# Performance work log

Hardware: AMD Instinct MI355X
Metric: run time of the kernel (lower is better)

Reference implementation:

```python
import jax, jax.numpy as jnp
import numpy as np

MIDC = 128
HEADS = 8
HEADC = MIDC // HEADS
EPS = 1e-5


def setup_inputs() -> dict:
    key = jax.random.key(0)
    ks = jax.random.split(key, 7)
    B, C, H, W = 8, MIDC, 128, 128
    x = jax.random.normal(ks[0], (B, C, H, W), dtype=jnp.float32)
    s = 1.0 / np.sqrt(C)
    qkv_w = jax.random.normal(ks[1], (3 * C, C), dtype=jnp.float32) * s
    qkv_b = jnp.zeros((3 * C,), dtype=jnp.float32)
    o1_w = jax.random.normal(ks[2], (C, C), dtype=jnp.float32) * s
    o1_b = jnp.zeros((C,), dtype=jnp.float32)
    o2_w = jax.random.normal(ks[3], (C, C), dtype=jnp.float32) * s
    o2_b = jnp.zeros((C,), dtype=jnp.float32)
    kln_w = jnp.ones((HEADS, 1, HEADC), dtype=jnp.float32)
    kln_b = jnp.zeros((HEADS, 1, HEADC), dtype=jnp.float32)
    vln_w = jnp.ones((HEADS, 1, HEADC), dtype=jnp.float32)
    vln_b = jnp.zeros((HEADS, 1, HEADC), dtype=jnp.float32)
    return {"x": x, "qkv_w": qkv_w, "qkv_b": qkv_b, "o1_w": o1_w, "o1_b": o1_b,
            "o2_w": o2_w, "o2_b": o2_b, "kln_w": kln_w, "kln_b": kln_b,
            "vln_w": vln_w, "vln_b": vln_b}


def _layernorm(t, w, b):
    # torch LayerNorm clone: mean/std over last dim, std uses ddof=1 (unbiased)
    mean = t.mean(-1, keepdims=True)
    std = jnp.std(t, axis=-1, ddof=1, keepdims=True)
    return w * ((t - mean) / (std + EPS)) + b


def reference(x, qkv_w, qkv_b, o1_w, o1_b, o2_w, o2_b, kln_w, kln_b, vln_w, vln_b):
    B, C, H, W = x.shape
    N = H * W
    bias0 = x
    # 1x1 conv == pointwise linear over channels
    xf = x.transpose(0, 2, 3, 1).reshape(B, N, C)              # [B, N, C]
    qkv = xf @ qkv_w.T + qkv_b                                 # [B, N, 3C]
    qkv = qkv.reshape(B, N, HEADS, 3 * HEADC).transpose(0, 2, 1, 3)  # [B, h, N, 3d]
    q, k, v = jnp.split(qkv, 3, axis=-1)                       # each [B, h, N, d]
    k = _layernorm(k, kln_w, kln_b)
    v = _layernorm(v, vln_w, vln_b)
    kv = jnp.einsum('bhnd,bhne->bhde', k, v) / N               # [B, h, d, d]
    av = jnp.einsum('bhnd,bhde->bhne', q, kv)                  # [B, h, N, d]
    av = av.transpose(0, 2, 1, 3).reshape(B, H, W, C)
    ret = av.transpose(0, 3, 1, 2) + bias0                     # [B, C, H, W]
    # o_proj1 -> GELU -> o_proj2, residual
    rf = ret.transpose(0, 2, 3, 1)                             # [B, H, W, C]
    h1 = jax.nn.gelu(rf @ o1_w.T + o1_b, approximate=False)
    h2 = h1 @ o2_w.T + o2_b
    return h2.transpose(0, 3, 1, 2) + bias0
```

## Files before the change

### kernel.cpp

```cpp
#include <hip/hip_runtime.h>
#include <hip/hip_bf16.h>

#define LN_EPS 1e-5f

typedef __bf16 bf16x8 __attribute__((ext_vector_type(8)));
typedef float  f32x4  __attribute__((ext_vector_type(4)));
typedef unsigned short u16;
typedef unsigned int u32;

__device__ __forceinline__ u16 f2bf(float f) {
    __bf16 b = (__bf16)f;
    return __builtin_bit_cast(u16, b);
}
__device__ __forceinline__ bf16x8 zero8() {
    bf16x8 v;
#pragma unroll
    for (int j = 0; j < 8; j++) v[j] = (__bf16)0.f;
    return v;
}
__device__ __forceinline__ float gelu_f(float v) {
    float t = v * fmaf(v * v, 0.0713548162726f, 1.5957691216057f);
    return v / (1.f + __expf(-t));
}

__global__ __launch_bounds__(256) void prep_kernel(
    const float* __restrict__ qkv_w, const float* __restrict__ o1_w,
    const float* __restrict__ o2_w, u16* __restrict__ wq,
    u16* __restrict__ o1f, u16* __restrict__ o2f) {
    int i = blockIdx.x * 256 + threadIdx.x;
    if (i >= 81920) return;
    int j = i;
    const float* src;
    u16* dst;
    if (j < 49152) { src = qkv_w; dst = wq; }
    else if (j < 65536) { j -= 49152; src = o1_w; dst = o1f; }
    else { j -= 65536; src = o2_w; dst = o2f; }
    int jj = j & 7;
    int l  = (j >> 3) & 63;
    int s  = (j >> 9) & 3;
    int t  = j >> 11;
    int outc = t * 16 + (l & 15);
    int k    = s * 32 + ((l >> 4) & 3) * 8 + jj;
    dst[j] = f2bf(src[outc * 128 + k]);
}

__global__ __launch_bounds__(512, 6) void k1(
    const float* __restrict__ x, const u16* __restrict__ wq,
    const float* __restrict__ qkv_b,
    const float* __restrict__ klw, const float* __restrict__ klb,
    const float* __restrict__ vlw, const float* __restrict__ vlb,
    u16* __restrict__ q_ws, float* __restrict__ part) {
    __shared__ __align__(16) char Rbuf[51200];
    u16* x_a  = (u16*)Rbuf;
    u16* kv_s = (u16*)Rbuf;
    u16* q_s  = (u16*)(Rbuf + 33792);
    u16* kT   = (u16*)Rbuf;
    u16* vT   = (u16*)(Rbuf + 18432);

    const int tid  = threadIdx.x;
    const int lane = tid & 63;
    const int wv   = tid >> 6;
    const int stripe = wv >> 1;
    const int half   = wv & 1;
    const int bid  = blockIdx.x;
    const int b    = bid >> 8;
    const int n0   = (bid & 255) * 64;

    {
        int cw  = tid & 63;
        int sub = tid >> 6;
        const float* p0 = x + ((size_t)(b * 128 + 2 * cw)) * 16384 + n0 + sub * 8;
        const float* p1 = p0 + 16384;
        float4 a0 = ((const float4*)p0)[0], a1 = ((const float4*)p0)[1];
        float4 c0 = ((const float4*)p1)[0], c1 = ((const float4*)p1)[1];
        float av[8] = {a0.x, a0.y, a0.z, a0.w, a1.x, a1.y, a1.z, a1.w};
        float cv[8] = {c0.x, c0.y, c0.z, c0.w, c1.x, c1.y, c1.z, c1.w};
        u32* dst = (u32*)x_a;
#pragma unroll
        for (int j = 0; j < 8; j++)
            dst[(sub * 8 + j) * 68 + cw] = (u32)f2bf(av[j]) | ((u32)f2bf(cv[j]) << 16);
    }
    __syncthreads();

    const int m16  = stripe * 16;
    const int l15  = lane & 15;
    const int quad = lane >> 4;

    bf16x8 af[4];
#pragma unroll
    for (int s = 0; s < 4; s++)
        af[s] = *(const bf16x8*)&x_a[(m16 + l15) * 136 + s * 32 + quad * 8];
    __syncthreads();

    const int tb = half * 12;
#pragma unroll
    for (int hh = 0; hh < 4; hh++) {
        const int tq = tb + 3 * hh;
        f32x4 aq  = (f32x4){0.f, 0.f, 0.f, 0.f};
        f32x4 ak  = (f32x4){0.f, 0.f, 0.f, 0.f};
        f32x4 avv = (f32x4){0.f, 0.f, 0.f, 0.f};
#pragma unroll
        for (int s = 0; s < 4; s++) {
            bf16x8 bq = *(const bf16x8*)(wq + (size_t)(((tq + 0) * 4 + s) * 64 + lane) * 8);
            bf16x8 bk = *(const bf16x8*)(wq + (size_t)(((tq + 1) * 4 + s) * 64 + lane) * 8);
            bf16x8 bv = *(const bf16x8*)(wq + (size_t)(((tq + 2) * 4 + s) * 64 + lane) * 8);
            aq  = __builtin_amdgcn_mfma_f32_16x16x32_bf16(af[s], bq, aq, 0, 0, 0);
            ak  = __builtin_amdgcn_mfma_f32_16x16x32_bf16(af[s], bk, ak, 0, 0, 0);
            avv = __builtin_amdgcn_mfma_f32_16x16x32_bf16(af[s], bv, avv, 0, 0, 0);
        }
        const int h = half * 4 + hh;
        float biasq = qkv_b[(tq + 0) * 16 + l15];
        float biask = qkv_b[(tq + 1) * 16 + l15];
        float biasv = qkv_b[(tq + 2) * 16 + l15];
#pragma unroll
        for (int r = 0; r < 4; r++) {
            int row = m16 + quad * 4 + r;
            q_s[row * 136 + h * 16 + l15]       = f2bf(aq[r] + biasq);
            kv_s[row * 264 + h * 32 + l15]      = f2bf(ak[r] + biask);
            kv_s[row * 264 + h * 32 + 16 + l15] = f2bf(avv[r] + biasv);
        }
    }
    __syncthreads();

    {
#pragma unroll
        for (int p = 0; p < 2; p++) {
            int c = tid + p * 512;
            int lane_c = c & 63;
            int s  = (c >> 6) & 3;
            int tl = c >> 8;
            int row = tl * 16 + (lane_c & 15);
            const uint4* src = (const uint4*)&q_s[row * 136 + s * 32 + (lane_c >> 4) * 8];
            size_t gtile = (size_t)b * 1024 + (n0 >> 4) + tl;
            *(uint4*)(q_ws + gtile * 2048 + s * 512 + lane_c * 8) = *src;
        }
    }
    const int hL = __builtin_amdgcn_readfirstlane(wv);
    const u16* rowp = &kv_s[lane * 264 + hL * 32];
    bf16x8 rk0 = *(const bf16x8*)(rowp);
    bf16x8 rk1 = *(const bf16x8*)(rowp + 8);
    bf16x8 rv0 = *(const bf16x8*)(rowp + 16);
    bf16x8 rv1 = *(const bf16x8*)(rowp + 24);
    __syncthreads();

    {
        float kf[16], vf[16];
#pragma unroll
        for (int j = 0; j < 8; j++) {
            kf[j] = (float)rk0[j]; kf[8 + j] = (float)rk1[j];
            vf[j] = (float)rv0[j]; vf[8 + j] = (float)rv1[j];
        }
        float ksum = 0.f, ksq = 0.f, vsum = 0.f, vsq = 0.f;
#pragma unroll
        for (int d = 0; d < 16; d++) {
            ksum += kf[d]; ksq = fmaf(kf[d], kf[d], ksq);
            vsum += vf[d]; vsq = fmaf(vf[d], vf[d], vsq);
        }
        float km = ksum * (1.f / 16.f);
        float kvar = (ksq - 16.f * km * km) * (1.f / 15.f);
        kvar = kvar < 0.f ? 0.f : kvar;
        float kinv = 1.f / (sqrtf(kvar) + LN_EPS);
        float vm = vsum * (1.f / 16.f);
        float vvar = (vsq - 16.f * vm * vm) * (1.f / 15.f);
        vvar = vvar < 0.f ? 0.f : vvar;
        float vinv = 1.f / (sqrtf(vvar) + LN_EPS);
        const float* kwp = klw + hL * 16; const float* kbp = klb + hL * 16;
        const float* vwp = vlw + hL * 16; const float* vbp = vlb + hL * 16;
#pragma unroll
        for (int d = 0; d < 16; d++) {
            kT[(hL * 16 + d) * 72 + lane] = f2bf(fmaf((kf[d] - km) * kinv, kwp[d], kbp[d]));
            vT[(hL * 16 + d) * 72 + lane] = f2bf(fmaf((vf[d] - vm) * vinv, vwp[d], vbp[d]));
        }
    }
    __syncthreads();

    {
        const u16* ka = &kT[(hL * 16 + l15) * 72 + quad * 8];
        const u16* vb = &vT[(hL * 16 + l15) * 72 + quad * 8];
        bf16x8 A0 = *(const bf16x8*)(ka);
        bf16x8 A1 = *(const bf16x8*)(ka + 32);
        bf16x8 B0 = *(const bf16x8*)(vb);
        bf16x8 B1 = *(const bf16x8*)(vb + 32);
        f32x4 kv = __builtin_amdgcn_mfma_f32_16x16x32_bf16(A0, B0, (f32x4){0.f,0.f,0.f,0.f}, 0, 0, 0);
        kv = __builtin_amdgcn_mfma_f32_16x16x32_bf16(A1, B1, kv, 0, 0, 0);
        ((f32x4*)part)[(size_t)(bid * 8 + hL) * 64 + lane] = kv;
    }
}

__global__ __launch_bounds__(256) void k_red(const float* __restrict__ part,
                                             u16* __restrict__ kvf) {
    __shared__ f32x4 red[4][64];
    const int tid  = threadIdx.x;
    const int lane = tid & 63;
    const int wvq  = tid >> 6;
    const int b = blockIdx.x >> 3;
    const int h = blockIdx.x & 7;

    const f32x4* p = (const f32x4*)part;
    f32x4 s = (f32x4){0.f, 0.f, 0.f, 0.f};
#pragma unroll 8
    for (int tt = 0; tt < 64; tt++) {
        int t = wvq * 64 + tt;
        f32x4 v = p[((size_t)(b * 256 + t) * 8 + h) * 64 + lane];
        s += v;
    }
    red[wvq][lane] = s;
    __syncthreads();
    if (tid < 64) {
        f32x4 tot = red[0][lane];
#pragma unroll
        for (int w = 1; w < 4; w++) tot += red[w][lane];
#pragma unroll
        for (int r = 0; r < 4; r++) {
            int dk = (lane >> 4) * 4 + r;
            int dv = lane & 15;
            kvf[(size_t)(b * 8 + h) * 256 + (dk >> 3) * 128 + dv * 8 + (dk & 7)] =
                f2bf(tot[r] * (1.f / 16384.f));
        }
    }
}

__global__ __launch_bounds__(256, 5) void k2(
    const float* __restrict__ x, const u16* __restrict__ q_ws,
    const u16* __restrict__ kvf, const u16* __restrict__ o1f,
    const u16* __restrict__ o2f, const float* __restrict__ o1_b,
    const float* __restrict__ o2_b, float* __restrict__ out) {
    __shared__ u16 a_s[32 * 136];
    __shared__ float x_s[128 * 36];

    const int tid  = threadIdx.x;
    const int lane = tid & 63;
    const int wv   = tid >> 6;
    const int stripe = wv >> 1;
    const int half   = wv & 1;
    const int bid  = blockIdx.x;
    const int b    = bid >> 9;
    const int n0   = (bid & 511) * 32;

    const int m16  = stripe * 16;
    const int l15  = lane & 15;
    const int quad = lane >> 4;
    const bool act = quad < 2;

    bf16x8 qf[4], kvb[4];
    {
        size_t gtile = (size_t)b * 1024 + (n0 >> 4) + stripe;
#pragma unroll
        for (int hh = 0; hh < 4; hh++) {
            int h = half * 4 + hh;
            if (act) {
                int laneq = ((h & 1) * 2 + quad) * 16 + l15;
                qf[hh]  = *(const bf16x8*)(q_ws + gtile * 2048 + (h >> 1) * 512 + laneq * 8);
                kvb[hh] = *(const bf16x8*)(kvf + (size_t)(b * 8 + h) * 256 + quad * 128 + l15 * 8);
            } else {
                qf[hh] = zero8(); kvb[hh] = zero8();
            }
        }
    }

    {
        int c = tid >> 1, nh = (tid & 1) * 16;
        const float4* xs = (const float4*)(x + ((size_t)(b * 128 + c)) * 16384 + n0 + nh);
        float4* xd = (float4*)&x_s[c * 36 + nh];
#pragma unroll
        for (int i = 0; i < 4; i++) xd[i] = xs[i];
    }
    __syncthreads();

#pragma unroll
    for (int hh = 0; hh < 4; hh++) {
        int h = half * 4 + hh;
        f32x4 acc = __builtin_amdgcn_mfma_f32_16x16x32_bf16(
            qf[hh], kvb[hh], (f32x4){0.f,0.f,0.f,0.f}, 0, 0, 0);
#pragma unroll
        for (int r = 0; r < 4; r++) {
            float rv = acc[r] + x_s[(h * 16 + l15) * 36 + m16 + quad * 4 + r];
            a_s[(m16 + quad * 4 + r) * 136 + h * 16 + l15] = f2bf(rv);
        }
    }
    __syncthreads();

    bf16x8 af2[4];
#pragma unroll
    for (int s = 0; s < 4; s++)
        af2[s] = *(const bf16x8*)&a_s[(m16 + l15) * 136 + s * 32 + quad * 8];
    f32x4 acc2[4];
#pragma unroll
    for (int t = 0; t < 4; t++) acc2[t] = (f32x4){0.f,0.f,0.f,0.f};
#pragma unroll
    for (int tt = 0; tt < 4; tt++) {
        int t = half * 4 + tt;
#pragma unroll
        for (int s = 0; s < 4; s++) {
            bf16x8 bf = *(const bf16x8*)(o1f + (size_t)((t * 4 + s) * 64 + lane) * 8);
            acc2[tt] = __builtin_amdgcn_mfma_f32_16x16x32_bf16(af2[s], bf, acc2[tt], 0, 0, 0);
        }
    }
    float g[4][4];
#pragma unroll
    for (int tt = 0; tt < 4; tt++) {
        float bb = o1_b[(half * 4 + tt) * 16 + l15];
#pragma unroll
        for (int r = 0; r < 4; r++)
            g[tt][r] = gelu_f(acc2[tt][r] + bb);
    }
    __syncthreads();
#pragma unroll
    for (int tt = 0; tt < 4; tt++)
#pragma unroll
        for (int r = 0; r < 4; r++)
            a_s[(m16 + quad * 4 + r) * 136 + (half * 4 + tt) * 16 + l15] = f2bf(g[tt][r]);
    __syncthreads();

#pragma unroll
    for (int s = 0; s < 4; s++)
        af2[s] = *(const bf16x8*)&a_s[(m16 + l15) * 136 + s * 32 + quad * 8];
#pragma unroll
    for (int t = 0; t < 4; t++) acc2[t] = (f32x4){0.f,0.f,0.f,0.f};
#pragma unroll
    for (int tt = 0; tt < 4; tt++) {
        int t = half * 4 + tt;
#pragma unroll
        for (int s = 0; s < 4; s++) {
            bf16x8 bf = *(const bf16x8*)(o2f + (size_t)((t * 4 + s) * 64 + lane) * 8);
            acc2[tt] = __builtin_amdgcn_mfma_f32_16x16x32_bf16(af2[s], bf, acc2[tt], 0, 0, 0);
        }
    }
#pragma unroll
    for (int tt = 0; tt < 4; tt++) {
        int t = half * 4 + tt;
        float bb = o2_b[t * 16 + l15];
#pragma unroll
        for (int r = 0; r < 4; r++) {
            int row = m16 + quad * 4 + r;
            int col = t * 16 + l15;
            x_s[col * 36 + row] = acc2[tt][r] + bb + x_s[col * 36 + row];
        }
    }
    __syncthreads();

    {
        int c = tid >> 1, nh = (tid & 1) * 16;
        float4* dst = (float4*)(out + ((size_t)(b * 128 + c)) * 16384 + n0 + nh);
        const float4* sv = (const float4*)&x_s[c * 36 + nh];
#pragma unroll
        for (int i = 0; i < 4; i++) dst[i] = sv[i];
    }
}

extern "C" void kernel_launch(void* const* d_in, const int* in_sizes, int n_in,
                              void* d_out, int out_size, void* d_ws, size_t ws_size,
                              hipStream_t stream) {
    (void)in_sizes; (void)n_in; (void)out_size; (void)ws_size;
    const float* x     = (const float*)d_in[0];
    const float* qkv_w = (const float*)d_in[1];
    const float* qkv_b = (const float*)d_in[2];
    const float* o1_w  = (const float*)d_in[3];
    const float* o1_b  = (const float*)d_in[4];
    const float* o2_w  = (const float*)d_in[5];
    const float* o2_b  = (const float*)d_in[6];
    const float* klw   = (const float*)d_in[7];
    const float* klb   = (const float*)d_in[8];
    const float* vlw   = (const float*)d_in[9];
    const float* vlb   = (const float*)d_in[10];
    float* outp = (float*)d_out;

    char* ws = (char*)d_ws;
    u16*   kvf  = (u16*)(ws);
    u16*   wq   = (u16*)(ws + 32768);
    u16*   o1f  = (u16*)(ws + 131072);
    u16*   o2f  = (u16*)(ws + 163840);
    float* part = (float*)(ws + 196608);
    u16*   q_ws = (u16*)(ws + 196608 + 16777216);

    prep_kernel<<<320, 256, 0, stream>>>(qkv_w, o1_w, o2_w, wq, o1f, o2f);
    k1<<<2048, 512, 0, stream>>>(x, wq, qkv_b, klw, klb, vlw, vlb, q_ws, part);
    k_red<<<64, 256, 0, stream>>>(part, kvf);
    k2<<<4096, 256, 0, stream>>>(x, q_ws, kvf, o1f, o2f, o1_b, o2_b, outp);
}
```

Before: 205.5 us.

## Split k1 into two 32-row subtiles per 256-thread block, accumulating kv in registers

The k1 kernel now launches 256-thread blocks that process each 64-row tile as two sequential 32-row subtiles. The per-head k^T v partial is accumulated in MFMA registers across both subtiles, and the LDS staging buffer is halved. The aim is to let more blocks reside per CU and improve latency hiding while keeping the same grid and partial-sum output. The cost is less parallelism inside each block and an extra barrier between subtiles. The LayerNorm work is also remapped so each wave handles two heads.

```diff
diff --git a/kernel.cpp b/kernel.cpp
--- a/kernel.cpp
+++ b/kernel.cpp
@@ -44,27 +44,27 @@
     dst[j] = f2bf(src[outc * 128 + k]);
 }
 
-__global__ __launch_bounds__(512, 6) void k1(
+__device__ __forceinline__ void k1_tile(
     const float* __restrict__ x, const u16* __restrict__ wq,
     const float* __restrict__ qkv_b,
     const float* __restrict__ klw, const float* __restrict__ klb,
     const float* __restrict__ vlw, const float* __restrict__ vlb,
-    u16* __restrict__ q_ws, float* __restrict__ part) {
-    __shared__ __align__(16) char Rbuf[51200];
+    u16* __restrict__ q_ws, char* Rbuf,
+    int b, int n0, f32x4* kvacc) {
     u16* x_a  = (u16*)Rbuf;
     u16* kv_s = (u16*)Rbuf;
-    u16* q_s  = (u16*)(Rbuf + 33792);
+    u16* q_s  = (u16*)(Rbuf + 16896);
     u16* kT   = (u16*)Rbuf;
-    u16* vT   = (u16*)(Rbuf + 18432);
+    u16* vT   = (u16*)(Rbuf + 10240);
 
     const int tid  = threadIdx.x;
     const int lane = tid & 63;
     const int wv   = tid >> 6;
     const int stripe = wv >> 1;
     const int half   = wv & 1;
-    const int bid  = blockIdx.x;
-    const int b    = bid >> 8;
-    const int n0   = (bid & 255) * 64;
+    const int m16  = stripe * 16;
+    const int l15  = lane & 15;
+    const int quad = lane >> 4;
 
     {
         int cw  = tid & 63;
@@ -82,10 +82,6 @@
     }
     __syncthreads();
 
-    const int m16  = stripe * 16;
-    const int l15  = lane & 15;
-    const int quad = lane >> 4;
-
     bf16x8 af[4];
 #pragma unroll
     for (int s = 0; s < 4; s++)
@@ -125,7 +121,7 @@
     {
 #pragma unroll
         for (int p = 0; p < 2; p++) {
-            int c = tid + p * 512;
+            int c = tid + p * 256;
             int lane_c = c & 63;
             int s  = (c >> 6) & 3;
             int tl = c >> 8;
@@ -135,8 +131,9 @@
             *(uint4*)(q_ws + gtile * 2048 + s * 512 + lane_c * 8) = *src;
         }
     }
-    const int hL = __builtin_amdgcn_readfirstlane(wv);
-    const u16* rowp = &kv_s[lane * 264 + hL * 32];
+    const int hL   = wv * 2 + (lane >> 5);
+    const int rown = lane & 31;
+    const u16* rowp = &kv_s[rown * 264 + hL * 32];
     bf16x8 rk0 = *(const bf16x8*)(rowp);
     bf16x8 rk1 = *(const bf16x8*)(rowp + 8);
     bf16x8 rv0 = *(const bf16x8*)(rowp + 16);
@@ -168,22 +165,49 @@
         const float* vwp = vlw + hL * 16; const float* vbp = vlb + hL * 16;
 #pragma unroll
         for (int d = 0; d < 16; d++) {
-            kT[(hL * 16 + d) * 72 + lane] = f2bf(fmaf((kf[d] - km) * kinv, kwp[d], kbp[d]));
-            vT[(hL * 16 + d) * 72 + lane] = f2bf(fmaf((vf[d] - vm) * vinv, vwp[d], vbp[d]));
-        }
-    }
-    __syncthreads();
-
-    {
-        const u16* ka = &kT[(hL * 16 + l15) * 72 + quad * 8];
-        const u16* vb = &vT[(hL * 16 + l15) * 72 + quad * 8];
+            kT[(hL * 16 + d) * 40 + rown] = f2bf(fmaf((kf[d] - km) * kinv, kwp[d], kbp[d]));
+            vT[(hL * 16 + d) * 40 + rown] = f2bf(fmaf((vf[d] - vm) * vinv, vwp[d], vbp[d]));
+        }
+    }
+    __syncthreads();
+
+#pragma unroll
+    for (int hh = 0; hh < 2; hh++) {
+        const int h = wv * 2 + hh;
+        const u16* ka = &kT[(h * 16 + l15) * 40 + quad * 8];
+        const u16* vb = &vT[(h * 16 + l15) * 40 + quad * 8];
         bf16x8 A0 = *(const bf16x8*)(ka);
-        bf16x8 A1 = *(const bf16x8*)(ka + 32);
         bf16x8 B0 = *(const bf16x8*)(vb);
-        bf16x8 B1 = *(const bf16x8*)(vb + 32);
-        f32x4 kv = __builtin_amdgcn_mfma_f32_16x16x32_bf16(A0, B0, (f32x4){0.f,0.f,0.f,0.f}, 0, 0, 0);
-        kv = __builtin_amdgcn_mfma_f32_16x16x32_bf16(A1, B1, kv, 0, 0, 0);
-        ((f32x4*)part)[(size_t)(bid * 8 + hL) * 64 + lane] = kv;
+        kvacc[hh] = __builtin_amdgcn_mfma_f32_16x16x32_bf16(A0, B0, kvacc[hh], 0, 0, 0);
+    }
+}
+
+__global__ __launch_bounds__(256, 6) void k1(
+    const float* __restrict__ x, const u16* __restrict__ wq,
+    const float* __restrict__ qkv_b,
+    const float* __restrict__ klw, const float* __restrict__ klb,
+    const float* __restrict__ vlw, const float* __restrict__ vlb,
+    u16* __restrict__ q_ws, float* __restrict__ part) {
+    __shared__ __align__(16) char Rbuf[25600];
+
+    const int bid  = blockIdx.x;
+    const int b    = bid >> 8;
+    const int tile0 = (bid & 255) * 64;
+    const int lane = threadIdx.x & 63;
+    const int wv   = threadIdx.x >> 6;
+
+    f32x4 kvacc[2];
+    kvacc[0] = (f32x4){0.f, 0.f, 0.f, 0.f};
+    kvacc[1] = (f32x4){0.f, 0.f, 0.f, 0.f};
+
+    k1_tile(x, wq, qkv_b, klw, klb, vlw, vlb, q_ws, Rbuf, b, tile0, kvacc);
+    __syncthreads();
+    k1_tile(x, wq, qkv_b, klw, klb, vlw, vlb, q_ws, Rbuf, b, tile0 + 32, kvacc);
+
+#pragma unroll
+    for (int hh = 0; hh < 2; hh++) {
+        const int h = wv * 2 + hh;
+        ((f32x4*)part)[(size_t)(bid * 8 + h) * 64 + lane] = kvacc[hh];
     }
 }
 
@@ -374,7 +398,7 @@
     u16*   q_ws = (u16*)(ws + 196608 + 16777216);
 
     prep_kernel<<<320, 256, 0, stream>>>(qkv_w, o1_w, o2_w, wq, o1f, o2f);
-    k1<<<2048, 512, 0, stream>>>(x, wq, qkv_b, klw, klb, vlw, vlb, q_ws, part);
+    k1<<<2048, 256, 0, stream>>>(x, wq, qkv_b, klw, klb, vlw, vlb, q_ws, part);
     k_red<<<64, 256, 0, stream>>>(part, kvf);
     k2<<<4096, 256, 0, stream>>>(x, q_ws, kvf, o1f, o2f, o1_b, o2_b, outp);
 }
```

New measurement: 358.4 us. 1.74x slower.

## Recompute Q projection inside the output kernel instead of staging it globally

Applied to the files above, without the earlier changes.

k1 now computes only K and V and no longer writes the bf16 Q tensor to a global workspace. k2 converts its x tile to bf16 in shared memory and runs the Q projection MFMAs itself, reusing the x tile it already loads for the residual. This drops a full-tensor global write and a full-tensor global read between the two kernels. In exchange k2 does extra MFMA work and uses more shared memory, and both kernels' launch-bounds occupancy hints change.

```diff
diff --git a/kernel.cpp b/kernel.cpp
--- a/kernel.cpp
+++ b/kernel.cpp
@@ -44,16 +44,15 @@
     dst[j] = f2bf(src[outc * 128 + k]);
 }
 
-__global__ __launch_bounds__(512, 6) void k1(
+__global__ __launch_bounds__(512, 8) void k1(
     const float* __restrict__ x, const u16* __restrict__ wq,
     const float* __restrict__ qkv_b,
     const float* __restrict__ klw, const float* __restrict__ klb,
     const float* __restrict__ vlw, const float* __restrict__ vlb,
-    u16* __restrict__ q_ws, float* __restrict__ part) {
-    __shared__ __align__(16) char Rbuf[51200];
+    float* __restrict__ part) {
+    __shared__ __align__(16) char Rbuf[36864];
     u16* x_a  = (u16*)Rbuf;
     u16* kv_s = (u16*)Rbuf;
-    u16* q_s  = (u16*)(Rbuf + 33792);
     u16* kT   = (u16*)Rbuf;
     u16* vT   = (u16*)(Rbuf + 18432);
 
@@ -96,45 +95,27 @@
 #pragma unroll
     for (int hh = 0; hh < 4; hh++) {
         const int tq = tb + 3 * hh;
-        f32x4 aq  = (f32x4){0.f, 0.f, 0.f, 0.f};
         f32x4 ak  = (f32x4){0.f, 0.f, 0.f, 0.f};
         f32x4 avv = (f32x4){0.f, 0.f, 0.f, 0.f};
 #pragma unroll
         for (int s = 0; s < 4; s++) {
-            bf16x8 bq = *(const bf16x8*)(wq + (size_t)(((tq + 0) * 4 + s) * 64 + lane) * 8);
             bf16x8 bk = *(const bf16x8*)(wq + (size_t)(((tq + 1) * 4 + s) * 64 + lane) * 8);
             bf16x8 bv = *(const bf16x8*)(wq + (size_t)(((tq + 2) * 4 + s) * 64 + lane) * 8);
-            aq  = __builtin_amdgcn_mfma_f32_16x16x32_bf16(af[s], bq, aq, 0, 0, 0);
             ak  = __builtin_amdgcn_mfma_f32_16x16x32_bf16(af[s], bk, ak, 0, 0, 0);
             avv = __builtin_amdgcn_mfma_f32_16x16x32_bf16(af[s], bv, avv, 0, 0, 0);
         }
         const int h = half * 4 + hh;
-        float biasq = qkv_b[(tq + 0) * 16 + l15];
         float biask = qkv_b[(tq + 1) * 16 + l15];
         float biasv = qkv_b[(tq + 2) * 16 + l15];
 #pragma unroll
         for (int r = 0; r < 4; r++) {
             int row = m16 + quad * 4 + r;
-            q_s[row * 136 + h * 16 + l15]       = f2bf(aq[r] + biasq);
             kv_s[row * 264 + h * 32 + l15]      = f2bf(ak[r] + biask);
             kv_s[row * 264 + h * 32 + 16 + l15] = f2bf(avv[r] + biasv);
         }
     }
     __syncthreads();
 
-    {
-#pragma unroll
-        for (int p = 0; p < 2; p++) {
-            int c = tid + p * 512;
-            int lane_c = c & 63;
-            int s  = (c >> 6) & 3;
-            int tl = c >> 8;
-            int row = tl * 16 + (lane_c & 15);
-            const uint4* src = (const uint4*)&q_s[row * 136 + s * 32 + (lane_c >> 4) * 8];
-            size_t gtile = (size_t)b * 1024 + (n0 >> 4) + tl;
-            *(uint4*)(q_ws + gtile * 2048 + s * 512 + lane_c * 8) = *src;
-        }
-    }
     const int hL = __builtin_amdgcn_readfirstlane(wv);
     const u16* rowp = &kv_s[lane * 264 + hL * 32];
     bf16x8 rk0 = *(const bf16x8*)(rowp);
@@ -220,13 +201,15 @@
     }
 }
 
-__global__ __launch_bounds__(256, 5) void k2(
-    const float* __restrict__ x, const u16* __restrict__ q_ws,
+__global__ __launch_bounds__(256, 4) void k2(
+    const float* __restrict__ x, const u16* __restrict__ wq,
+    const float* __restrict__ qkv_b,
     const u16* __restrict__ kvf, const u16* __restrict__ o1f,
     const u16* __restrict__ o2f, const float* __restrict__ o1_b,
     const float* __restrict__ o2_b, float* __restrict__ out) {
     __shared__ u16 a_s[32 * 136];
     __shared__ float x_s[128 * 36];
+    __shared__ u16 x_a16[32 * 136];
 
     const int tid  = threadIdx.x;
     const int lane = tid & 63;
@@ -242,30 +225,67 @@
     const int quad = lane >> 4;
     const bool act = quad < 2;
 
-    bf16x8 qf[4], kvb[4];
-    {
-        size_t gtile = (size_t)b * 1024 + (n0 >> 4) + stripe;
+    bf16x8 kvb[4];
+    {
 #pragma unroll
         for (int hh = 0; hh < 4; hh++) {
             int h = half * 4 + hh;
             if (act) {
-                int laneq = ((h & 1) * 2 + quad) * 16 + l15;
-                qf[hh]  = *(const bf16x8*)(q_ws + gtile * 2048 + (h >> 1) * 512 + laneq * 8);
                 kvb[hh] = *(const bf16x8*)(kvf + (size_t)(b * 8 + h) * 256 + quad * 128 + l15 * 8);
             } else {
-                qf[hh] = zero8(); kvb[hh] = zero8();
+                kvb[hh] = zero8();
             }
         }
     }
 
     {
-        int c = tid >> 1, nh = (tid & 1) * 16;
-        const float4* xs = (const float4*)(x + ((size_t)(b * 128 + c)) * 16384 + n0 + nh);
-        float4* xd = (float4*)&x_s[c * 36 + nh];
-#pragma unroll
-        for (int i = 0; i < 4; i++) xd[i] = xs[i];
-    }
-    __syncthreads();
+        int cw  = tid & 63;
+        int sub = tid >> 6;
+        const float* p0 = x + ((size_t)(b * 128 + 2 * cw)) * 16384 + n0 + sub * 8;
+        const float* p1 = p0 + 16384;
+        float4 a0 = ((const float4*)p0)[0], a1 = ((const float4*)p0)[1];
+        float4 c0 = ((const float4*)p1)[0], c1 = ((const float4*)p1)[1];
+        float av[8] = {a0.x, a0.y, a0.z, a0.w, a1.x, a1.y, a1.z, a1.w};
+        float cv[8] = {c0.x, c0.y, c0.z, c0.w, c1.x, c1.y, c1.z, c1.w};
+        u32* da = (u32*)x_a16;
+#pragma unroll
+        for (int j = 0; j < 8; j++)
+            da[(sub * 8 + j) * 68 + cw] = (u32)f2bf(av[j]) | ((u32)f2bf(cv[j]) << 16);
+        float4* q0 = (float4*)&x_s[(2 * cw) * 36 + sub * 8];
+        q0[0] = a0; q0[1] = a1;
+        float4* q1 = (float4*)&x_s[(2 * cw + 1) * 36 + sub * 8];
+        q1[0] = c0; q1[1] = c1;
+    }
+    __syncthreads();
+
+    {
+        bf16x8 axf[4];
+#pragma unroll
+        for (int s = 0; s < 4; s++)
+            axf[s] = *(const bf16x8*)&x_a16[(m16 + l15) * 136 + s * 32 + quad * 8];
+#pragma unroll
+        for (int hh = 0; hh < 4; hh++) {
+            int h = half * 4 + hh;
+            int tq = 3 * h;
+            f32x4 aq = (f32x4){0.f, 0.f, 0.f, 0.f};
+#pragma unroll
+            for (int s = 0; s < 4; s++) {
+                bf16x8 bq = *(const bf16x8*)(wq + (size_t)((tq * 4 + s) * 64 + lane) * 8);
+                aq = __builtin_amdgcn_mfma_f32_16x16x32_bf16(axf[s], bq, aq, 0, 0, 0);
+            }
+            float biasq = qkv_b[tq * 16 + l15];
+#pragma unroll
+            for (int r = 0; r < 4; r++)
+                a_s[(m16 + quad * 4 + r) * 136 + h * 16 + l15] = f2bf(aq[r] + biasq);
+        }
+    }
+    bf16x8 qf[4];
+#pragma unroll
+    for (int hh = 0; hh < 4; hh++) {
+        int h = half * 4 + hh;
+        if (act) qf[hh] = *(const bf16x8*)&a_s[(m16 + l15) * 136 + h * 16 + quad * 8];
+        else     qf[hh] = zero8();
+    }
 
 #pragma unroll
     for (int hh = 0; hh < 4; hh++) {
@@ -371,10 +391,9 @@
     u16*   o1f  = (u16*)(ws + 131072);
     u16*   o2f  = (u16*)(ws + 163840);
     float* part = (float*)(ws + 196608);
-    u16*   q_ws = (u16*)(ws + 196608 + 16777216);
 
     prep_kernel<<<320, 256, 0, stream>>>(qkv_w, o1_w, o2_w, wq, o1f, o2f);
-    k1<<<2048, 512, 0, stream>>>(x, wq, qkv_b, klw, klb, vlw, vlb, q_ws, part);
+    k1<<<2048, 512, 0, stream>>>(x, wq, qkv_b, klw, klb, vlw, vlb, part);
     k_red<<<64, 256, 0, stream>>>(part, kvf);
-    k2<<<4096, 256, 0, stream>>>(x, q_ws, kvf, o1f, o2f, o1_b, o2_b, outp);
-}
+    k2<<<4096, 256, 0, stream>>>(x, wq, qkv_b, kvf, o1f, o2f, o1_b, o2_b, outp);
+}
```

Measured after the change: 211.9 us. +3.1%, slower.
